# Kernel tuning notes

Hardware: AMD Instinct MI355X
Metric: run time of the kernel (lower is better)

The kernel has to match this reference:

```python
import jax, jax.numpy as jnp
import numpy as np

B, T, D, H, DK = 4, 1024, 512, 8, 64
L = 2 * T - 1  # relative position length
EPS = 1e-3     # keras LayerNormalization default epsilon


def rel_shift(x, klen):
    # x: [B, H, T, L] with L = 2T-1 -> [B, H, T, klen] (Transformer-XL shift)
    b, h, t, l = x.shape
    x = x.reshape(b, h, l, t)[:, :, 1:, :]
    x = x.reshape(b, h, t, l - 1)
    return x[:, :, :, :klen]


def setup_inputs() -> dict:
    key = jax.random.key(0)
    ks = jax.random.split(key, 16)
    s = 0.02
    return {
        "x": jax.random.normal(ks[0], (B, T, D), jnp.float32),
        "pos": jax.random.normal(ks[1], (B, L, D), jnp.float32),
        "content_bias": jax.random.normal(ks[2], (H, DK), jnp.float32) * s,
        "pos_bias": jax.random.normal(ks[3], (H, DK), jnp.float32) * s,
        "gamma": jnp.ones((D,), jnp.float32),
        "beta": jnp.zeros((D,), jnp.float32),
        "Wq": jax.random.normal(ks[4], (D, H, DK), jnp.float32) * s,
        "bq": jnp.zeros((H, DK), jnp.float32),
        "Wk": jax.random.normal(ks[5], (D, H, DK), jnp.float32) * s,
        "bk": jnp.zeros((H, DK), jnp.float32),
        "Wv": jax.random.normal(ks[6], (D, H, DK), jnp.float32) * s,
        "bv": jnp.zeros((H, DK), jnp.float32),
        "Wp": jax.random.normal(ks[7], (D, H, DK), jnp.float32) * s,
        "Wo": jax.random.normal(ks[8], (H, DK, D), jnp.float32) * s,
        "bo": jnp.zeros((D,), jnp.float32),
    }


def reference(x, pos, content_bias, pos_bias, gamma, beta,
              Wq, bq, Wk, bk, Wv, bv, Wp, Wo, bo):
    # pre-norm LayerNorm
    mean = jnp.mean(x, axis=-1, keepdims=True)
    var = jnp.var(x, axis=-1, keepdims=True)
    y = (x - mean) * jax.lax.rsqrt(var + EPS) * gamma + beta

    # per-head projections
    q = jnp.einsum("bid,dhk->bihk", y, Wq) + bq      # [B,T,H,DK]
    k = jnp.einsum("bjd,dhk->bjhk", y, Wk) + bk
    v = jnp.einsum("bjd,dhk->bjhk", y, Wv) + bv
    p = jnp.einsum("bld,dhk->blhk", pos, Wp)          # [B,L,H,DK], no bias

    # Transformer-XL content + positional scores
    content = jnp.einsum("bihk,bjhk->bhij", q + content_bias, k)   # [B,H,T,T]
    positional = jnp.einsum("bihk,blhk->bhil", q + pos_bias, p)    # [B,H,T,L]
    positional = rel_shift(positional, content.shape[-1])          # [B,H,T,T]

    scores = (content + positional) / np.sqrt(DK).astype(np.float32)
    attn = jax.nn.softmax(scores, axis=-1)

    o = jnp.einsum("bhij,bjhk->bihk", attn, v)       # [B,T,H,DK]
    out = jnp.einsum("bihk,hkd->bid", o, Wo) + bo    # [B,T,D]

    # dropout is identity at inference; residual with factor=1.0
    return x + out
```

## Files before the change

kernel.cpp:

```cpp
#include <hip/hip_runtime.h>
#include <hip/hip_bf16.h>

typedef __hip_bfloat16 bf16;
typedef __attribute__((ext_vector_type(8))) short short8;
typedef __attribute__((ext_vector_type(4))) float f32x4;

#define B_  4
#define T_  1024
#define D_  512
#define H_  8
#define DK_ 64
#define L_  2047

__device__ __forceinline__ float b2f(bf16 v) { return __bfloat162float(v); }
__device__ __forceinline__ bf16  f2b(float v) { return __float2bfloat16(v); }
__device__ __forceinline__ float bits2f(unsigned short u) {
    return __uint_as_float(((unsigned int)u) << 16);
}
__device__ __forceinline__ unsigned short fbits(float v) {
    bf16 h = f2b(v); return *(unsigned short*)&h;
}

#define MFMA16(a, b, c) __builtin_amdgcn_mfma_f32_16x16x32_bf16(a, b, c, 0, 0, 0)
#define GLD_LDS16(g, l) __builtin_amdgcn_global_load_lds( \
    (const __attribute__((address_space(1))) unsigned int*)(g), \
    (__attribute__((address_space(3))) unsigned int*)(l), 16, 0, 0)

__global__ __launch_bounds__(256) void prep_all(
        const float* __restrict__ Wq, const float* __restrict__ Wk,
        const float* __restrict__ Wv, const float* __restrict__ Wp,
        const float* __restrict__ Wo,
        const float* __restrict__ bq, const float* __restrict__ bk,
        const float* __restrict__ bv,
        const float* __restrict__ pos, const float* __restrict__ x,
        const float* __restrict__ gamma, const float* __restrict__ beta,
        bf16* __restrict__ Wqkv_t, bf16* __restrict__ Wp_t, bf16* __restrict__ Wo_t,
        float* __restrict__ biasq, bf16* __restrict__ pos_bf, bf16* __restrict__ y) {
    __shared__ float tl[32][33];
    __shared__ float ws1[4], ws2[4];
    const int blk = blockIdx.x;
    const int t = threadIdx.x;

    if (blk < 1280) {
        const int z = blk >> 8, rem = blk & 255;
        const float* W; bf16* Wt; int roff;
        switch (z) {
            case 0: W = Wq; Wt = Wqkv_t; roff = 0;    break;
            case 1: W = Wk; Wt = Wqkv_t; roff = 512;  break;
            case 2: W = Wv; Wt = Wqkv_t; roff = 1024; break;
            case 3: W = Wp; Wt = Wp_t;   roff = 0;    break;
            default: W = Wo; Wt = Wo_t;  roff = 0;    break;
        }
        const int n0 = (rem & 15) * 32, k0 = (rem >> 4) * 32;
        const int tx = t & 31, ty = t >> 5;
#pragma unroll
        for (int r = 0; r < 4; ++r)
            tl[ty + r * 8][tx] = W[(size_t)(k0 + ty + r * 8) * 512 + n0 + tx];
        __syncthreads();
#pragma unroll
        for (int r = 0; r < 4; ++r)
            Wt[(size_t)(roff + n0 + ty + r * 8) * 512 + k0 + tx] = f2b(tl[tx][ty + r * 8]);
    } else if (blk < 1286) {
        int i = (blk - 1280) * 256 + t;
        biasq[i] = (i < 512) ? bq[i] : (i < 1024) ? bk[i - 512] : bv[i - 1024];
    } else if (blk < 3333) {
        size_t i = ((size_t)(blk - 1286) * 256 + t) * 8;
        float4 a = *(const float4*)(pos + i);
        float4 c = *(const float4*)(pos + i + 4);
        uint4 wv;
        wv.x = ((unsigned)fbits(a.y) << 16) | fbits(a.x);
        wv.y = ((unsigned)fbits(a.w) << 16) | fbits(a.z);
        wv.z = ((unsigned)fbits(c.y) << 16) | fbits(c.x);
        wv.w = ((unsigned)fbits(c.w) << 16) | fbits(c.z);
        *(uint4*)((unsigned short*)pos_bf + i) = wv;
    } else {
        const int row = blk - 3333;
        const float* xr = x + (size_t)row * D_;
        float v0 = xr[t];
        float v1 = xr[t + 256];
        float s  = v0 + v1;
        float s2 = v0 * v0 + v1 * v1;
#pragma unroll
        for (int off = 32; off > 0; off >>= 1) {
            s  += __shfl_down(s,  off, 64);
            s2 += __shfl_down(s2, off, 64);
        }
        const int wid = t >> 6, lane = t & 63;
        if (!lane) { ws1[wid] = s; ws2[wid] = s2; }
        __syncthreads();
        float S  = ws1[0] + ws1[1] + ws1[2] + ws1[3];
        float S2 = ws2[0] + ws2[1] + ws2[2] + ws2[3];
        float mean = S * (1.f / D_);
        float var  = S2 * (1.f / D_) - mean * mean;
        float r = rsqrtf(var + 1e-3f);
        bf16* yr = y + (size_t)row * D_;
        yr[t]       = f2b((v0 - mean) * r * gamma[t]       + beta[t]);
        yr[t + 256] = f2b((v1 - mean) * r * gamma[t + 256] + beta[t + 256]);
    }
}

__device__ __forceinline__ void gemm_body(
        const bf16* __restrict__ A, const bf16* __restrict__ Wt,
        const float* __restrict__ bias,
        bf16* __restrict__ C, int M, size_t seg_elems, int m0, int n0,
        unsigned short (*A_s)[32], unsigned short (*B_s)[32]) {
    const int t = threadIdx.x;
    const int w = t >> 6, lane = t & 63;
    const int quad = lane >> 4, n16 = lane & 15;
    const int wm = (w >> 1) * 64, wn = (w & 1) * 64;

    f32x4 acc[4][4];
#pragma unroll
    for (int a = 0; a < 4; ++a)
#pragma unroll
        for (int b = 0; b < 4; ++b) acc[a][b] = (f32x4){0.f, 0.f, 0.f, 0.f};

    const int ar = lane >> 2, ac8 = (lane & 3) * 8;
    auto stage = [&](int k0, int buf) {
        const int bo = buf << 7;
#pragma unroll
        for (int ps = 0; ps < 2; ++ps) {
            int br = (ps * 4 + w) * 16;
            GLD_LDS16(A  + (size_t)(m0 + br + ar) * 512 + k0 + ac8, &A_s[bo + br][0]);
            GLD_LDS16(Wt + (size_t)(n0 + br + ar) * 512 + k0 + ac8, &B_s[bo + br][0]);
        }
    };
    stage(0, 0);
    int cur = 0;
    for (int k0 = 0; k0 < 512; k0 += 32) {
        __syncthreads();
        if (k0 + 32 < 512) stage(k0 + 32, cur ^ 1);
        const int bo = cur << 7;
        short8 af[4], bfr[4];
#pragma unroll
        for (int i = 0; i < 4; ++i) {
            af[i]  = *(const short8*)&A_s[bo + wm + i * 16 + n16][quad * 8];
            bfr[i] = *(const short8*)&B_s[bo + wn + i * 16 + n16][quad * 8];
        }
#pragma unroll
        for (int mi = 0; mi < 4; ++mi)
#pragma unroll
            for (int ni = 0; ni < 4; ++ni)
                acc[mi][ni] = MFMA16(af[mi], bfr[ni], acc[mi][ni]);
        cur ^= 1;
    }

    const int seg = n0 >> 9;
#pragma unroll
    for (int mi = 0; mi < 4; ++mi) {
#pragma unroll
        for (int r = 0; r < 4; ++r) {
            int row = m0 + wm + mi * 16 + quad * 4 + r;
            if (row >= M) continue;
#pragma unroll
            for (int ni = 0; ni < 4; ++ni) {
                int col  = n0 + wn + ni * 16 + n16;
                int coll = col & 511;
                float vv = acc[mi][ni][r];
                if (bias) vv += bias[col];
                bf16* Cp = C + seg * seg_elems;
                Cp[(size_t)row * 512 + coll] = f2b(vv);
            }
        }
    }
}

__global__ __launch_bounds__(256) void gemm_qkvp(
        const bf16* __restrict__ y, const bf16* __restrict__ pos_bf,
        const bf16* __restrict__ Wqkv_t, const bf16* __restrict__ Wp_t,
        const float* __restrict__ biasq,
        bf16* __restrict__ q, bf16* __restrict__ p, size_t seg_elems) {
    __shared__ __align__(16) unsigned short A_s[256][32];
    __shared__ __align__(16) unsigned short B_s[256][32];
    const int gid = blockIdx.x;
    if (gid < 384) {
        const int xcd = gid & 7, s = gid >> 3;
        const int n = s % 12;
        const int m = xcd * 4 + s / 12;
        gemm_body(y, Wqkv_t, biasq, q, 4096, seg_elems, m * 128, n * 128, A_s, B_s);
    } else {
        const int g2 = gid - 384;
        const int xcd = g2 & 7, s = g2 >> 3;
        const int n = s & 3;
        const int m = xcd * 8 + (s >> 2);
        gemm_body(pos_bf, Wp_t, nullptr, p, 8188, 0, m * 128, n * 128, A_s, B_s);
    }
}

__global__ __launch_bounds__(256) void gemm_out(
        const bf16* __restrict__ o, const bf16* __restrict__ Wo_t,
        const float* __restrict__ bo, const float* __restrict__ x,
        float* __restrict__ out) {
    __shared__ __align__(16) unsigned short A_s[128][32];
    __shared__ __align__(16) unsigned short B_s[256][32];
    const int gid = blockIdx.x;
    const int xcd = gid & 7, s = gid >> 3;
    const int n0 = (s & 3) * 128;
    const int m0 = (xcd * 8 + (s >> 2)) * 64;
    const int t = threadIdx.x;
    const int w = t >> 6, lane = t & 63;
    const int quad = lane >> 4, n16 = lane & 15;
    const int wm = (w >> 1) * 32, wn = (w & 1) * 64;

    f32x4 acc[2][4];
#pragma unroll
    for (int a = 0; a < 2; ++a)
#pragma unroll
        for (int b = 0; b < 4; ++b) acc[a][b] = (f32x4){0.f, 0.f, 0.f, 0.f};

    const int ar = lane >> 2, ac8 = (lane & 3) * 8;
    auto stage = [&](int k0, int buf) {
        GLD_LDS16(o + (size_t)(m0 + w * 16 + ar) * 512 + k0 + ac8,
                  &A_s[buf * 64 + w * 16][0]);
#pragma unroll
        for (int ps = 0; ps < 2; ++ps)
            GLD_LDS16(Wo_t + (size_t)(n0 + (ps * 4 + w) * 16 + ar) * 512 + k0 + ac8,
                      &B_s[buf * 128 + (ps * 4 + w) * 16][0]);
    };
    stage(0, 0);
    int cur = 0;
    for (int k0 = 0; k0 < 512; k0 += 32) {
        __syncthreads();
        if (k0 + 32 < 512) stage(k0 + 32, cur ^ 1);
        short8 af[2], bfr[4];
#pragma unroll
        for (int i = 0; i < 2; ++i)
            af[i] = *(const short8*)&A_s[cur * 64 + wm + i * 16 + n16][quad * 8];
#pragma unroll
        for (int i = 0; i < 4; ++i)
            bfr[i] = *(const short8*)&B_s[cur * 128 + wn + i * 16 + n16][quad * 8];
#pragma unroll
        for (int mi = 0; mi < 2; ++mi)
#pragma unroll
            for (int ni = 0; ni < 4; ++ni)
                acc[mi][ni] = MFMA16(af[mi], bfr[ni], acc[mi][ni]);
        cur ^= 1;
    }
#pragma unroll
    for (int mi = 0; mi < 2; ++mi) {
#pragma unroll
        for (int r = 0; r < 4; ++r) {
            int row = m0 + wm + mi * 16 + quad * 4 + r;
#pragma unroll
            for (int ni = 0; ni < 4; ++ni) {
                int col = n0 + wn + ni * 16 + n16;
                out[(size_t)row * 512 + col] =
                    acc[mi][ni][r] + bo[col] + x[(size_t)row * 512 + col];
            }
        }
    }
}

__global__ __launch_bounds__(256, 2) void attn_mfma_kernel(
        const bf16* __restrict__ q, const bf16* __restrict__ k,
        const bf16* __restrict__ v, const bf16* __restrict__ p,
        const float* __restrict__ cbias, const float* __restrict__ pbias,
        bf16* __restrict__ o) {
    __shared__ __align__(16) unsigned short k_s[2][4096];
    __shared__ __align__(16) unsigned short pw_s[3][4096];
    __shared__ __align__(16) unsigned short vt_s[2][64][72];
    __shared__ __align__(16) unsigned short gbuf[4][16][72];
    __shared__ float cb_s[64], pb_s[64];
    __shared__ float wrap_s;

    const int i0 = blockIdx.x * 64;
    const int h  = blockIdx.y;
    const int b  = blockIdx.z;
    const int t  = threadIdx.x;
    const int w    = t >> 6;
    const int lane = t & 63;
    const int quad = lane >> 4;
    const int n16  = lane & 15;
    const int h64  = h * 64;
    const float sc_scale = 0.125f * 1.4426950408889634f;

    if (t < 64)       cb_s[t]      = cbias[h64 + t];
    else if (t < 128) pb_s[t - 64] = pbias[h64 + t - 64];

    const int l8 = lane >> 3, l7 = lane & 7;
    const int clog8 = (l7 ^ l8) * 8;
    const unsigned short* ksrc[2];
    const unsigned short* psrc[2];
#pragma unroll
    for (int ps = 0; ps < 2; ++ps) {
        int row = (w * 2 + ps) * 8 + l8;
        ksrc[ps] = (const unsigned short*)k + ((size_t)(b * T_ + row) * 512 + h64 + clog8);
    }
    const int slb = T_ - i0 - 63;
#pragma unroll
    for (int ps = 0; ps < 2; ++ps) {
        int row = (w * 2 + ps) * 8 + l8;
        psrc[ps] = (const unsigned short*)p + ((size_t)(b * L_ + slb + row) * 512 + h64 + clog8);
    }
    auto stageP = [&](int c) {
        size_t joff = (size_t)c * 64 * 512;
#pragma unroll
        for (int ps = 0; ps < 2; ++ps)
            GLD_LDS16(psrc[ps] + joff, &pw_s[c % 3][(w * 2 + ps) * 512]);
    };
    auto stage = [&](int n) {
        size_t joff = (size_t)n * 64 * 512;
#pragma unroll
        for (int ps = 0; ps < 2; ++ps)
            GLD_LDS16(ksrc[ps] + joff, &k_s[n & 1][(w * 2 + ps) * 512]);
        stageP(n + 1);
    };

    const int vd2 = (t & 31) * 2, vjg = t >> 5;
    const unsigned short* vsrc = (const unsigned short*)v +
        ((size_t)(b * T_ + vjg * 8) * 512 + h64 + vd2);
    unsigned int vReg[8];
    auto vload = [&](int j0n) {
        const unsigned short* vg = vsrc + (size_t)j0n * 512;
#pragma unroll
        for (int e = 0; e < 8; ++e) vReg[e] = *(const unsigned int*)(vg + (size_t)e * 512);
    };
    auto vwrite = [&](int nxt) {
        uint4 wlo, whi;
        wlo.x = (vReg[0] & 0xffffu) | (vReg[1] << 16);
        wlo.y = (vReg[2] & 0xffffu) | (vReg[3] << 16);
        wlo.z = (vReg[4] & 0xffffu) | (vReg[5] << 16);
        wlo.w = (vReg[6] & 0xffffu) | (vReg[7] << 16);
        whi.x = (vReg[0] >> 16) | (vReg[1] & 0xffff0000u);
        whi.y = (vReg[2] >> 16) | (vReg[3] & 0xffff0000u);
        whi.z = (vReg[4] >> 16) | (vReg[5] & 0xffff0000u);
        whi.w = (vReg[6] >> 16) | (vReg[7] & 0xffff0000u);
        *(uint4*)&vt_s[nxt][vd2][vjg * 8]     = wlo;
        *(uint4*)&vt_s[nxt][vd2 + 1][vjg * 8] = whi;
    };

    stageP(0);
    stage(0);
    vload(0);
    __syncthreads();

    short8 ac[2], ap[2];
    {
        const unsigned short* qrow = (const unsigned short*)q +
            ((size_t)(b * T_ + i0 + 16 * w + n16) * 512 + h64);
#pragma unroll
        for (int kc = 0; kc < 2; ++kc) {
            uint4 u = *(const uint4*)(qrow + kc * 32 + quad * 8);
            const unsigned short* uv = (const unsigned short*)&u;
            unsigned short* acp = (unsigned short*)&ac[kc];
            unsigned short* app = (unsigned short*)&ap[kc];
#pragma unroll
            for (int e = 0; e < 8; ++e) {
                int d = kc * 32 + quad * 8 + e;
                float qv = bits2f(uv[e]);
                acp[e] = fbits((qv + cb_s[d]) * sc_scale);
                app[e] = fbits((qv + pb_s[d]) * sc_scale);
            }
        }
    }
    if (i0 == 0 && t < 64) {
        float part = (b2f(q[(size_t)(b * T_ + 1) * 512 + h64 + t]) + pb_s[t]) *
                     b2f(p[(size_t)(b * L_) * 512 + h64 + t]);
#pragma unroll
        for (int m = 1; m < 64; m <<= 1) part += __shfl_xor(part, m, 64);
        if (t == 0) wrap_s = part * sc_scale;
    }

    int srcl[4]; bool hi_[4];
#pragma unroll
    for (int r = 0; r < 4; ++r) {
        int ii = quad * 4 + r;
        srcl[r] = (lane & 48) | ((n16 - ii - 1) & 15);
        hi_[r]  = n16 > ii;
    }
    short8 onesb;
    {
        const short ov = (n16 == 0) ? (short)0x3F80 : (short)0;
#pragma unroll
        for (int e = 0; e < 8; ++e) onesb[e] = ov;
    }

    const int swzA = (quad ^ (n16 & 7)) * 16;
    const int swzB = swzA ^ 64;

    f32x4 O[4], O4;
#pragma unroll
    for (int nt = 0; nt < 4; ++nt) O[nt] = (f32x4){0.f, 0.f, 0.f, 0.f};
    O4 = (f32x4){0.f, 0.f, 0.f, 0.f};

    auto qk = [&](f32x4 (&Sc)[4], f32x4 (&G)[5], int tn) {
        const int buf = tn & 1;
        const char* krA = (const char*)&k_s[buf][0] + n16 * 128 + swzA;
        const char* krB = (const char*)&k_s[buf][0] + n16 * 128 + swzB;
        const char* pbank[2] = { (const char*)&pw_s[tn % 3][0],
                                 (const char*)&pw_s[(tn + 1) % 3][0] };
#pragma unroll
        for (int nt = 0; nt < 4; ++nt) Sc[nt] = (f32x4){0.f, 0.f, 0.f, 0.f};
#pragma unroll
        for (int ct = 0; ct < 5; ++ct) G[ct] = (f32x4){0.f, 0.f, 0.f, 0.f};
        __builtin_amdgcn_s_setprio(1);
#pragma unroll
        for (int kc = 0; kc < 2; ++kc) {
#pragma unroll
            for (int nt = 0; nt < 4; ++nt) {
                short8 bk = *(const short8*)((kc ? krB : krA) + nt * 2048);
                Sc[nt] = MFMA16(ac[kc], bk, Sc[nt]);
            }
#pragma unroll
            for (int ct = 0; ct < 5; ++ct) {
                const int gi = 3 - w + ct;
                const char* pr = pbank[gi >> 2] +
                    ((gi & 3) * 16 + n16) * 128 + (kc ? swzB : swzA);
                short8 bp = *(const short8*)pr;
                G[ct] = MFMA16(ap[kc], bp, G[ct]);
            }
        }
        __builtin_amdgcn_s_setprio(0);
    };

    auto sm_pv = [&](const f32x4 (&Sc)[4], const f32x4 (&G)[5], int vb, bool dowrap) {
        float pe[4][4];
#pragma unroll
        for (int r = 0; r < 4; ++r) {
            float s0 = __shfl(G[0][r], srcl[r], 64);
            float s1 = __shfl(G[1][r], srcl[r], 64);
            float s2 = __shfl(G[2][r], srcl[r], 64);
            float s3 = __shfl(G[3][r], srcl[r], 64);
            float s4 = __shfl(G[4][r], srcl[r], 64);
            pe[0][r] = Sc[0][r] + (hi_[r] ? s1 : s0);
            pe[1][r] = Sc[1][r] + (hi_[r] ? s2 : s1);
            pe[2][r] = Sc[2][r] + (hi_[r] ? s3 : s2);
            pe[3][r] = Sc[3][r] + (hi_[r] ? s4 : s3);
        }
        if (dowrap && i0 == 0 && w == 0 && lane == 15)
            pe[3][0] = Sc[3][0] + wrap_s;
#pragma unroll
        for (int ct = 0; ct < 4; ++ct)
#pragma unroll
            for (int r = 0; r < 4; ++r)
                *(bf16*)&gbuf[w][quad * 4 + r][ct * 16 + n16] = f2b(exp2f(pe[ct][r]));
        __builtin_amdgcn_s_setprio(1);
#pragma unroll
        for (int kc = 0; kc < 2; ++kc) {
            short8 pa = *(const short8*)&gbuf[w][n16][kc * 32 + quad * 8];
#pragma unroll
            for (int nt = 0; nt < 4; ++nt) {
                short8 vb8 = *(const short8*)&vt_s[vb][nt * 16 + n16][kc * 32 + quad * 8];
                O[nt] = MFMA16(pa, vb8, O[nt]);
            }
            O4 = MFMA16(pa, onesb, O4);
        }
        __builtin_amdgcn_s_setprio(0);
    };

    f32x4 ScA[4], GA[5], ScB[4], GB[5];

    vwrite(0);
    stage(1);
    vload(64);
    qk(ScA, GA, 0);

    auto body = [&](int tt, f32x4 (&ScC)[4], f32x4 (&GC)[5],
                    const f32x4 (&ScP)[4], const f32x4 (&GP)[5], bool more) {
        __syncthreads();
        vwrite(tt & 1);
        if (more) { stage(tt + 1); vload((tt + 1) * 64); }
        qk(ScC, GC, tt);
        sm_pv(ScP, GP, (tt - 1) & 1, false);
    };

#pragma unroll
    for (int tp = 0; tp < 7; ++tp) {
        body(2 * tp + 1, ScB, GB, ScA, GA, true);
        body(2 * tp + 2, ScA, GA, ScB, GB, true);
    }
    body(15, ScB, GB, ScA, GA, false);

    __syncthreads();
    sm_pv(ScB, GB, 1, true);

#pragma unroll
    for (int r = 0; r < 4; ++r) {
        float l = __shfl(O4[r], lane & 48, 64);
        float inv = 1.f / l;
        int row = i0 + 16 * w + quad * 4 + r;
#pragma unroll
        for (int nt = 0; nt < 4; ++nt)
            o[(size_t)(b * T_ + row) * 512 + h64 + nt * 16 + n16] = f2b(O[nt][r] * inv);
    }
}

extern "C" void kernel_launch(void* const* d_in, const int* in_sizes, int n_in,
                              void* d_out, int out_size, void* d_ws, size_t ws_size,
                              hipStream_t stream) {
    (void)in_sizes; (void)n_in; (void)out_size;
    const float* x     = (const float*)d_in[0];
    const float* pos   = (const float*)d_in[1];
    const float* cb    = (const float*)d_in[2];
    const float* pb    = (const float*)d_in[3];
    const float* gamma = (const float*)d_in[4];
    const float* beta  = (const float*)d_in[5];
    const float* Wq    = (const float*)d_in[6];
    const float* bq    = (const float*)d_in[7];
    const float* Wk    = (const float*)d_in[8];
    const float* bk    = (const float*)d_in[9];
    const float* Wv    = (const float*)d_in[10];
    const float* bv    = (const float*)d_in[11];
    const float* Wp    = (const float*)d_in[12];
    const float* Wo    = (const float*)d_in[13];
    const float* bo    = (const float*)d_in[14];
    float* out = (float*)d_out;

    const int BT = B_ * T_;

    const size_t sz_bt = (size_t)BT * D_;
    const size_t sz_bl = (size_t)(B_ * L_) * D_;
    const size_t sz_w  = 512 * 512;
    const size_t need  = (5 * sz_bt + sz_bl + 5 * sz_w) * sizeof(bf16) + 1536 * sizeof(float);
    if (ws_size < need) return;

    bf16* y       = (bf16*)d_ws;
    bf16* o       = y + sz_bt;
    bf16* q       = y + 2 * sz_bt;
    bf16* k       = y + 3 * sz_bt;
    bf16* v       = y + 4 * sz_bt;
    bf16* p       = y + 5 * sz_bt;
    bf16* Wqkv_t  = p + sz_bl;
    bf16* Wp_t    = Wqkv_t + 3 * sz_w;
    bf16* Wo_t    = Wp_t + sz_w;
    float* biasq  = (float*)(Wo_t + sz_w);
    bf16* pos_bf  = (bf16*)d_out;

    prep_all<<<7429, 256, 0, stream>>>(Wq, Wk, Wv, Wp, Wo, bq, bk, bv, pos, x,
                                       gamma, beta, Wqkv_t, Wp_t, Wo_t, biasq, pos_bf, y);

    gemm_qkvp<<<640, 256, 0, stream>>>(y, pos_bf, Wqkv_t, Wp_t, biasq, q, p, sz_bt);

    attn_mfma_kernel<<<dim3(T_ / 64, H_, B_), 256, 0, stream>>>(q, k, v, p, cb, pb, o);

    gemm_out<<<256, 256, 0, stream>>>(o, Wo_t, bo, x, out);
}
```

Baseline: 185.7 us.

## Double K-step depth in projection GEMM and restage P as 128-row windows

The projection GEMM now stages 64-wide K slices per barrier instead of 32, which halves the number of loop iterations and __syncthreads calls at the cost of twice the LDS. In the attention kernel, the positional tile ring of three 64-row buffers is replaced by two 128-row buffers, each loaded directly per tile. This simplifies the address arithmetic for the shifted P reads, using a fixed per-wave offset instead of computed bank indices, but it loads each P row twice across adjacent tiles. The extra LDS in both kernels may lower occupancy.

```diff
diff --git a/kernel.cpp b/kernel.cpp
--- a/kernel.cpp
+++ b/kernel.cpp
@@ -117,31 +117,38 @@
 
     const int ar = lane >> 2, ac8 = (lane & 3) * 8;
     auto stage = [&](int k0, int buf) {
-        const int bo = buf << 7;
-#pragma unroll
-        for (int ps = 0; ps < 2; ++ps) {
-            int br = (ps * 4 + w) * 16;
-            GLD_LDS16(A  + (size_t)(m0 + br + ar) * 512 + k0 + ac8, &A_s[bo + br][0]);
-            GLD_LDS16(Wt + (size_t)(n0 + br + ar) * 512 + k0 + ac8, &B_s[bo + br][0]);
-        }
+        const int bo = buf << 8;
+#pragma unroll
+        for (int kc = 0; kc < 2; ++kc)
+#pragma unroll
+            for (int ps = 0; ps < 2; ++ps) {
+                int br = (ps * 4 + w) * 16;
+                GLD_LDS16(A  + (size_t)(m0 + br + ar) * 512 + k0 + kc * 32 + ac8,
+                          &A_s[bo + kc * 128 + br][0]);
+                GLD_LDS16(Wt + (size_t)(n0 + br + ar) * 512 + k0 + kc * 32 + ac8,
+                          &B_s[bo + kc * 128 + br][0]);
+            }
     };
     stage(0, 0);
     int cur = 0;
-    for (int k0 = 0; k0 < 512; k0 += 32) {
+    for (int k0 = 0; k0 < 512; k0 += 64) {
         __syncthreads();
-        if (k0 + 32 < 512) stage(k0 + 32, cur ^ 1);
-        const int bo = cur << 7;
-        short8 af[4], bfr[4];
-#pragma unroll
-        for (int i = 0; i < 4; ++i) {
-            af[i]  = *(const short8*)&A_s[bo + wm + i * 16 + n16][quad * 8];
-            bfr[i] = *(const short8*)&B_s[bo + wn + i * 16 + n16][quad * 8];
-        }
-#pragma unroll
-        for (int mi = 0; mi < 4; ++mi)
-#pragma unroll
-            for (int ni = 0; ni < 4; ++ni)
-                acc[mi][ni] = MFMA16(af[mi], bfr[ni], acc[mi][ni]);
+        if (k0 + 64 < 512) stage(k0 + 64, cur ^ 1);
+        const int bo = cur << 8;
+#pragma unroll
+        for (int kc = 0; kc < 2; ++kc) {
+            short8 af[4], bfr[4];
+#pragma unroll
+            for (int i = 0; i < 4; ++i) {
+                af[i]  = *(const short8*)&A_s[bo + kc * 128 + wm + i * 16 + n16][quad * 8];
+                bfr[i] = *(const short8*)&B_s[bo + kc * 128 + wn + i * 16 + n16][quad * 8];
+            }
+#pragma unroll
+            for (int mi = 0; mi < 4; ++mi)
+#pragma unroll
+                for (int ni = 0; ni < 4; ++ni)
+                    acc[mi][ni] = MFMA16(af[mi], bfr[ni], acc[mi][ni]);
+        }
         cur ^= 1;
     }
 
@@ -170,8 +177,8 @@
         const bf16* __restrict__ Wqkv_t, const bf16* __restrict__ Wp_t,
         const float* __restrict__ biasq,
         bf16* __restrict__ q, bf16* __restrict__ p, size_t seg_elems) {
-    __shared__ __align__(16) unsigned short A_s[256][32];
-    __shared__ __align__(16) unsigned short B_s[256][32];
+    __shared__ __align__(16) unsigned short A_s[512][32];
+    __shared__ __align__(16) unsigned short B_s[512][32];
     const int gid = blockIdx.x;
     if (gid < 384) {
         const int xcd = gid & 7, s = gid >> 3;
@@ -257,7 +264,7 @@
         const float* __restrict__ cbias, const float* __restrict__ pbias,
         bf16* __restrict__ o) {
     __shared__ __align__(16) unsigned short k_s[2][4096];
-    __shared__ __align__(16) unsigned short pw_s[3][4096];
+    __shared__ __align__(16) unsigned short pw_s[2][8192];
     __shared__ __align__(16) unsigned short vt_s[2][64][72];
     __shared__ __align__(16) unsigned short gbuf[4][16][72];
     __shared__ float cb_s[64], pb_s[64];
@@ -280,7 +287,7 @@
     const int l8 = lane >> 3, l7 = lane & 7;
     const int clog8 = (l7 ^ l8) * 8;
     const unsigned short* ksrc[2];
-    const unsigned short* psrc[2];
+    const unsigned short* psrc[4];
 #pragma unroll
     for (int ps = 0; ps < 2; ++ps) {
         int row = (w * 2 + ps) * 8 + l8;
@@ -288,22 +295,18 @@
     }
     const int slb = T_ - i0 - 63;
 #pragma unroll
-    for (int ps = 0; ps < 2; ++ps) {
-        int row = (w * 2 + ps) * 8 + l8;
+    for (int ps = 0; ps < 4; ++ps) {
+        int row = (w * 4 + ps) * 8 + l8;
         psrc[ps] = (const unsigned short*)p + ((size_t)(b * L_ + slb + row) * 512 + h64 + clog8);
     }
-    auto stageP = [&](int c) {
-        size_t joff = (size_t)c * 64 * 512;
+    auto stage = [&](int j0n, int nxt) {
+        size_t joff = (size_t)j0n * 512;
 #pragma unroll
         for (int ps = 0; ps < 2; ++ps)
-            GLD_LDS16(psrc[ps] + joff, &pw_s[c % 3][(w * 2 + ps) * 512]);
-    };
-    auto stage = [&](int n) {
-        size_t joff = (size_t)n * 64 * 512;
-#pragma unroll
-        for (int ps = 0; ps < 2; ++ps)
-            GLD_LDS16(ksrc[ps] + joff, &k_s[n & 1][(w * 2 + ps) * 512]);
-        stageP(n + 1);
+            GLD_LDS16(ksrc[ps] + joff, &k_s[nxt][(w * 2 + ps) * 512]);
+#pragma unroll
+        for (int ps = 0; ps < 4; ++ps)
+            GLD_LDS16(psrc[ps] + joff, &pw_s[nxt][(w * 4 + ps) * 512]);
     };
 
     const int vd2 = (t & 31) * 2, vjg = t >> 5;
@@ -329,8 +332,7 @@
         *(uint4*)&vt_s[nxt][vd2 + 1][vjg * 8] = whi;
     };
 
-    stageP(0);
-    stage(0);
+    stage(0, 0);
     vload(0);
     __syncthreads();
 
@@ -375,20 +377,20 @@
         for (int e = 0; e < 8; ++e) onesb[e] = ov;
     }
 
-    const int swzA = (quad ^ (n16 & 7)) * 16;
-    const int swzB = swzA ^ 64;
+    const int pwoff = 48 - 16 * w;
+    const int swzA  = (quad ^ (n16 & 7)) * 16;
+    const int swzB  = swzA ^ 64;
 
     f32x4 O[4], O4;
 #pragma unroll
     for (int nt = 0; nt < 4; ++nt) O[nt] = (f32x4){0.f, 0.f, 0.f, 0.f};
     O4 = (f32x4){0.f, 0.f, 0.f, 0.f};
 
-    auto qk = [&](f32x4 (&Sc)[4], f32x4 (&G)[5], int tn) {
-        const int buf = tn & 1;
-        const char* krA = (const char*)&k_s[buf][0] + n16 * 128 + swzA;
-        const char* krB = (const char*)&k_s[buf][0] + n16 * 128 + swzB;
-        const char* pbank[2] = { (const char*)&pw_s[tn % 3][0],
-                                 (const char*)&pw_s[(tn + 1) % 3][0] };
+    auto qk = [&](f32x4 (&Sc)[4], f32x4 (&G)[5], int buf) {
+        const char* krA  = (const char*)&k_s[buf][0]  + n16 * 128 + swzA;
+        const char* krB  = (const char*)&k_s[buf][0]  + n16 * 128 + swzB;
+        const char* pwrA = (const char*)&pw_s[buf][0] + (pwoff + n16) * 128 + swzA;
+        const char* pwrB = (const char*)&pw_s[buf][0] + (pwoff + n16) * 128 + swzB;
 #pragma unroll
         for (int nt = 0; nt < 4; ++nt) Sc[nt] = (f32x4){0.f, 0.f, 0.f, 0.f};
 #pragma unroll
@@ -403,10 +405,7 @@
             }
 #pragma unroll
             for (int ct = 0; ct < 5; ++ct) {
-                const int gi = 3 - w + ct;
-                const char* pr = pbank[gi >> 2] +
-                    ((gi & 3) * 16 + n16) * 128 + (kc ? swzB : swzA);
-                short8 bp = *(const short8*)pr;
+                short8 bp = *(const short8*)((kc ? pwrB : pwrA) + ct * 2048);
                 G[ct] = MFMA16(ap[kc], bp, G[ct]);
             }
         }
@@ -451,7 +450,7 @@
     f32x4 ScA[4], GA[5], ScB[4], GB[5];
 
     vwrite(0);
-    stage(1);
+    stage(64, 1);
     vload(64);
     qk(ScA, GA, 0);
 
@@ -459,8 +458,8 @@
                     const f32x4 (&ScP)[4], const f32x4 (&GP)[5], bool more) {
         __syncthreads();
         vwrite(tt & 1);
-        if (more) { stage(tt + 1); vload((tt + 1) * 64); }
-        qk(ScC, GC, tt);
+        if (more) { stage((tt + 1) * 64, (tt + 1) & 1); vload((tt + 1) * 64); }
+        qk(ScC, GC, tt & 1);
         sm_pv(ScP, GP, (tt - 1) & 1, false);
     };
 
```

New measurement: 176.3 us. 5.1% less time.
